# Optimization experiments

Hardware: AMD Instinct MI355X
Metric: run time of the kernel (lower is better)

Reference implementation:

```python
import jax, jax.numpy as jnp
import numpy as np

B = 1024            # number of graphs
C = (64, 32, 16, 1) # args.channels
K = 25              # args.kernel_size
CUTOFF = 0.5        # args.cutoff
EPS = 1e-15


def gmm_conv(x, pos, n, g, mu, sigma, root, bias, out_ch):
    """GMMConv over a dynamically-built radius graph (dist<CUTOFF, no self loops),
    with mean aggregation, expressed densely per-graph (n in {5,25,75}).
    Equivalent to getA()+PyG GMMConv(aggr='mean') scatter/gather."""
    nb = pos.shape[0] // n
    posb = pos.reshape(nb, n, 2)
    # diff[b, s, t] = pos_t - pos_s  (edge (row=s, col=t): message flows s -> t)
    diff = posb[:, None, :, :] - posb[:, :, None, :]
    dist = jnp.linalg.norm(diff + 1e-12, axis=-1)            # [B,n,n]
    mask = (dist < CUTOFF) & (~jnp.eye(n, dtype=bool))       # [B,n,n]
    pseudo = diff / CUTOFF + 0.5                             # [B,n,n,2] edge_attr
    # Gaussian kernel weights: exp(-0.5 * sum_d (u_d - mu_kd)^2 / sigma_kd^2)
    gauss = jnp.exp(-0.5 * jnp.sum((pseudo[..., None, :] - mu) ** 2
                                   / (sigma ** 2 + EPS), axis=-1))  # [B,n,n,K]
    w = gauss * mask[..., None]
    xm = (x @ g).reshape(nb, n, K, out_ch)                   # source-transformed feats
    agg = jnp.einsum('bstk,bsko->bto', w, xm)                # scatter-sum into targets
    deg = jnp.maximum(jnp.sum(mask, axis=1), 1)              # in-degree per target [B,n]
    out = agg / deg[..., None].astype(x.dtype)               # mean aggregation
    return out.reshape(-1, out_ch) + x @ root + bias


def setup_inputs() -> dict:
    key = jax.random.key(0)
    ks = jax.random.split(key, 40)
    inp = {}
    inp['x'] = jax.random.normal(ks[0], (B * 5, C[0]), jnp.float32)
    inp['pos'] = jax.random.uniform(ks[1], (B * 5, 2), jnp.float32)

    def conv_params(k, fin, fout):
        k1, k2, k3, k4, k5 = jax.random.split(k, 5)
        g = jax.random.normal(k1, (fin, K * fout), jnp.float32) / np.sqrt(fin)
        mu = jax.random.normal(k2, (K, 2), jnp.float32)
        sigma = jax.random.uniform(k3, (K, 2), jnp.float32, minval=0.5, maxval=1.5)
        root = jax.random.normal(k4, (fin, fout), jnp.float32) / np.sqrt(fin)
        bias = jax.random.normal(k5, (fout,), jnp.float32) * 0.01
        return g, mu, sigma, root, bias

    for i, (fin, fout) in enumerate([(C[0], 5 * C[1]), (C[1], 3 * C[2]), (C[2], C[3])], 1):
        g, mu, sigma, root, bias = conv_params(ks[1 + i], fin, fout)
        inp[f'g{i}'], inp[f'mu{i}'], inp[f'sig{i}'] = g, mu, sigma
        inp[f'root{i}'], inp[f'cb{i}'] = root, bias

    def lin(k, fin, fout):
        kw, kb = jax.random.split(k)
        return (jax.random.normal(kw, (fin, fout), jnp.float32) / np.sqrt(fin),
                jax.random.normal(kb, (fout,), jnp.float32) * 0.01)

    for j, (pre, dims) in enumerate([('p1', (2 + C[1], 128, 64, 2)),
                                     ('p2', (2 + C[2], 128, 64, 2))]):
        for li in range(3):
            w, b_ = lin(ks[10 + 3 * j + li], dims[li], dims[li + 1])
            inp[f'{pre}w{li+1}'], inp[f'{pre}b{li+1}'] = w, b_
    return inp


def reference(x, pos, g1, mu1, sig1, root1, cb1, g2, mu2, sig2, root2, cb2,
              g3, mu3, sig3, root3, cb3,
              p1w1, p1b1, p1w2, p1b2, p1w3, p1b3,
              p2w1, p2b1, p2w2, p2b2, p2w3, p2b3):
    elu = jax.nn.elu
    # stage 1: 5 nodes/graph, conv expands node count x5
    x = elu(gmm_conv(x, pos, 5, g1, mu1, sig1, root1, cb1, 5 * C[1])).reshape(-1, C[1])
    p = jnp.concatenate([jnp.repeat(pos, 5, axis=0), x], axis=1)
    p = elu(p @ p1w1 + p1b1)
    p = elu(p @ p1w2 + p1b2)
    pos = elu(p @ p1w3 + p1b3)
    # stage 2: 25 nodes/graph, conv expands node count x3
    x = elu(gmm_conv(x, pos, 25, g2, mu2, sig2, root2, cb2, 3 * C[2])).reshape(-1, C[2])
    p = jnp.concatenate([jnp.repeat(pos, 3, axis=0), x], axis=1)
    p = elu(p @ p2w1 + p2b1)
    p = elu(p @ p2w2 + p2b2)
    pos = elu(p @ p2w3 + p2b3)
    # stage 3: 75 nodes/graph
    x = jnp.tanh(gmm_conv(x, pos, 75, g3, mu3, sig3, root3, cb3, C[3])).reshape(-1, C[3])
    return x, pos
```

## Files before the change

kernel.cpp:

```cpp
#include <hip/hip_runtime.h>
#include <math.h>


__device__ __forceinline__ float eluf(float v) { return v > 0.f ? v : __expf(v) - 1.f; }

#define NLOG2E_HALF (-0.72134752f)

#define FMA4(A, S, V) \
  A.x = fmaf(S, V.x, A.x); A.y = fmaf(S, V.y, A.y); \
  A.z = fmaf(S, V.z, A.z); A.w = fmaf(S, V.w, A.w);

#define C1G(J, XV) \
  a[J][0]=fmaf(XV.x,gv0.x,a[J][0]); a[J][1]=fmaf(XV.x,gv0.y,a[J][1]); a[J][2]=fmaf(XV.x,gv0.z,a[J][2]); a[J][3]=fmaf(XV.x,gv0.w,a[J][3]); \
  a[J][0]=fmaf(XV.y,gv1.x,a[J][0]); a[J][1]=fmaf(XV.y,gv1.y,a[J][1]); a[J][2]=fmaf(XV.y,gv1.z,a[J][2]); a[J][3]=fmaf(XV.y,gv1.w,a[J][3]); \
  a[J][0]=fmaf(XV.z,gv2.x,a[J][0]); a[J][1]=fmaf(XV.z,gv2.y,a[J][1]); a[J][2]=fmaf(XV.z,gv2.z,a[J][2]); a[J][3]=fmaf(XV.z,gv2.w,a[J][3]); \
  a[J][0]=fmaf(XV.w,gv3.x,a[J][0]); a[J][1]=fmaf(XV.w,gv3.y,a[J][1]); a[J][2]=fmaf(XV.w,gv3.z,a[J][2]); a[J][3]=fmaf(XV.w,gv3.w,a[J][3]);

__global__ __launch_bounds__(512) void conv1_kernel(
    const float* __restrict__ x, const float* __restrict__ pos,
    const float* __restrict__ g, const float* __restrict__ mu, const float* __restrict__ sig,
    const float* __restrict__ root, const float* __restrict__ bias,
    float* __restrict__ xout)
{
  const int b = blockIdx.x, tid = threadIdx.x;
  __shared__ __align__(16) float s_xT[64 * 12];
  __shared__ __align__(16) float s_xm[10 * 832];
  __shared__ __align__(16) float s_w[2 * 5 * 5 * 28];
  __shared__ __align__(16) float s_red[2 * 2 * 5 * 160];
  __shared__ float s_pos[20];
  __shared__ float s_msc[25][4];
  __shared__ float s_ideg[10];

  if (tid < 20) s_pos[tid] = pos[b * 20 + tid];
  if (tid < 25) {
    float m0 = mu[2 * tid], m1 = mu[2 * tid + 1];
    float s0 = sig[2 * tid], s1 = sig[2 * tid + 1];
    s_msc[tid][0] = 0.5f - m0;
    s_msc[tid][1] = 0.5f - m1;
    s_msc[tid][2] = NLOG2E_HALF / (s0 * s0 + 1e-15f);
    s_msc[tid][3] = NLOG2E_HALF / (s1 * s1 + 1e-15f);
  }
  for (int e = tid; e < 640; e += 512) { int nd = e >> 6, i = e & 63; s_xT[i * 12 + nd] = x[b * 640 + nd * 64 + i]; }
  for (int e = tid; e < 320; e += 512) { int r = e / 32, c = e % 32; s_xm[r * 832 + 800 + c] = 0.f; }
  __syncthreads();

  if (tid < 10) {
    int gg = tid / 5, t = tid % 5, c = 0;
    for (int s = 0; s < 5; ++s) {
      if (s == t) continue;
      float d0 = s_pos[(gg * 5 + t) * 2]     - s_pos[(gg * 5 + s) * 2]     + 1e-12f;
      float d1 = s_pos[(gg * 5 + t) * 2 + 1] - s_pos[(gg * 5 + s) * 2 + 1] + 1e-12f;
      c += (d0 * d0 + d1 * d1 < 0.25f) ? 1 : 0;
    }
    s_ideg[tid] = 1.f / (float)(c < 1 ? 1 : c);
  }
  for (int e = tid; e < 1400; e += 512) {
    int gg = e / 700, r2 = e % 700, t = r2 / 140, c = r2 % 140;
    int ch = c / 28, skl = c % 28;
    float wv = 0.f;
    if (skl < 25) {
      int kk = skl / 5, s = skl % 5, k = ch * 5 + kk;
      float d0 = s_pos[(gg * 5 + t) * 2]     - s_pos[(gg * 5 + s) * 2];
      float d1 = s_pos[(gg * 5 + t) * 2 + 1] - s_pos[(gg * 5 + s) * 2 + 1];
      float e0 = d0 + 1e-12f, e1 = d1 + 1e-12f;
      bool m = (e0 * e0 + e1 * e1 < 0.25f) && (s != t);
      float q0 = fmaf(2.f, d0, s_msc[k][0]);
      float q1 = fmaf(2.f, d1, s_msc[k][1]);
      float a = q0 * q0 * s_msc[k][2];
      a = fmaf(q1 * q1, s_msc[k][3], a);
      wv = m ? exp2f(a) : 0.f;
    }
    s_w[e] = wv;
  }
  __syncthreads();

  float sacc[5][2];
  #pragma unroll
  for (int t = 0; t < 5; ++t) { sacc[t][0] = 0.f; sacc[t][1] = 0.f; }
  const int sg = tid / 160, sr = tid % 160, sks = sr / 80, sob = sr % 80;
  const int so0 = sob * 2;

  for (int ch = 0; ch < 5; ++ch) {
    if (tid < 400) {
      const int c0 = tid * 2;
      const float* gp = g + ch * 800 + c0;
      float a[10][2];
      #pragma unroll
      for (int r = 0; r < 10; ++r) { a[r][0] = 0.f; a[r][1] = 0.f; }
      #pragma unroll 4
      for (int i = 0; i < 64; ++i) {
        float2 gv = *(const float2*)(gp + i * 4000);
        float4 xa = *(const float4*)&s_xT[i * 12];
        float4 xb = *(const float4*)&s_xT[i * 12 + 4];
        float2 xc = *(const float2*)&s_xT[i * 12 + 8];
        a[0][0] = fmaf(xa.x, gv.x, a[0][0]); a[0][1] = fmaf(xa.x, gv.y, a[0][1]);
        a[1][0] = fmaf(xa.y, gv.x, a[1][0]); a[1][1] = fmaf(xa.y, gv.y, a[1][1]);
        a[2][0] = fmaf(xa.z, gv.x, a[2][0]); a[2][1] = fmaf(xa.z, gv.y, a[2][1]);
        a[3][0] = fmaf(xa.w, gv.x, a[3][0]); a[3][1] = fmaf(xa.w, gv.y, a[3][1]);
        a[4][0] = fmaf(xb.x, gv.x, a[4][0]); a[4][1] = fmaf(xb.x, gv.y, a[4][1]);
        a[5][0] = fmaf(xb.y, gv.x, a[5][0]); a[5][1] = fmaf(xb.y, gv.y, a[5][1]);
        a[6][0] = fmaf(xb.z, gv.x, a[6][0]); a[6][1] = fmaf(xb.z, gv.y, a[6][1]);
        a[7][0] = fmaf(xb.w, gv.x, a[7][0]); a[7][1] = fmaf(xb.w, gv.y, a[7][1]);
        a[8][0] = fmaf(xc.x, gv.x, a[8][0]); a[8][1] = fmaf(xc.x, gv.y, a[8][1]);
        a[9][0] = fmaf(xc.y, gv.x, a[9][0]); a[9][1] = fmaf(xc.y, gv.y, a[9][1]);
      }
      #pragma unroll
      for (int r = 0; r < 10; ++r)
        *(float2*)&s_xm[r * 832 + c0] = make_float2(a[r][0], a[r][1]);
    }
    __syncthreads();
    if (tid < 320) {
#define C1_STEP(SK0) { \
      float2 m0 = *(const float2*)&s_xm[(sg * 5 + ((SK0) % 5)) * 832 + ((SK0) / 5) * 160 + so0]; \
      float2 m1 = *(const float2*)&s_xm[(sg * 5 + (((SK0) + 1) % 5)) * 832 + (((SK0) + 1) / 5) * 160 + so0]; \
      float2 m2 = *(const float2*)&s_xm[(sg * 5 + (((SK0) + 2) % 5)) * 832 + (((SK0) + 2) / 5) * 160 + so0]; \
      float2 m3 = *(const float2*)&s_xm[(sg * 5 + (((SK0) + 3) % 5)) * 832 + (((SK0) + 3) / 5) * 160 + so0]; \
      _Pragma("unroll") \
      for (int t = 0; t < 5; ++t) { \
        const float4 wv = *(const float4*)&s_w[((sg * 5 + t) * 5 + ch) * 28 + (SK0)]; \
        sacc[t][0] = fmaf(wv.x, m0.x, sacc[t][0]); sacc[t][1] = fmaf(wv.x, m0.y, sacc[t][1]); \
        sacc[t][0] = fmaf(wv.y, m1.x, sacc[t][0]); sacc[t][1] = fmaf(wv.y, m1.y, sacc[t][1]); \
        sacc[t][0] = fmaf(wv.z, m2.x, sacc[t][0]); sacc[t][1] = fmaf(wv.z, m2.y, sacc[t][1]); \
        sacc[t][0] = fmaf(wv.w, m3.x, sacc[t][0]); sacc[t][1] = fmaf(wv.w, m3.y, sacc[t][1]); \
      } }
      if (sks == 0) { C1_STEP(0) C1_STEP(4) C1_STEP(8) C1_STEP(12) }
      else          { C1_STEP(16) C1_STEP(20) C1_STEP(24) }
#undef C1_STEP
    }
    __syncthreads();
  }

  if (tid < 400) {
    const int rb = tid / 80, cb = tid % 80;
    const int r0 = rb * 2, c0 = cb * 2;
    float a00 = 0.f, a01 = 0.f, a10 = 0.f, a11 = 0.f;
    #pragma unroll 4
    for (int i = 0; i < 64; ++i) {
      float2 rv = *(const float2*)(root + i * 160 + c0);
      float2 xv = *(const float2*)&s_xT[i * 12 + r0];
      a00 = fmaf(xv.x, rv.x, a00); a01 = fmaf(xv.x, rv.y, a01);
      a10 = fmaf(xv.y, rv.x, a10); a11 = fmaf(xv.y, rv.y, a11);
    }
    *(float2*)&s_xm[r0 * 832 + c0]       = make_float2(a00, a01);
    *(float2*)&s_xm[(r0 + 1) * 832 + c0] = make_float2(a10, a11);
  }
  if (tid < 320) {
    #pragma unroll
    for (int t = 0; t < 5; ++t) {
      s_red[((sks * 2 + sg) * 5 + t) * 160 + so0]     = sacc[t][0];
      s_red[((sks * 2 + sg) * 5 + t) * 160 + so0 + 1] = sacc[t][1];
    }
  }
  __syncthreads();
  for (int e = tid; e < 1600; e += 512) {
    int gg = e / 800, r2 = e % 800, t = r2 / 160, o = r2 % 160;
    float v = s_red[(gg * 5 + t) * 160 + o] + s_red[((2 + gg) * 5 + t) * 160 + o];
    v = v * s_ideg[gg * 5 + t] + s_xm[(gg * 5 + t) * 832 + o] + bias[o];
    xout[b * 1600 + e] = eluf(v);
  }
}

__global__ __launch_bounds__(320) void conv2_kernel(
    const float* __restrict__ x, const float* __restrict__ pos,
    const float* __restrict__ g, const float* __restrict__ mu, const float* __restrict__ sig,
    const float* __restrict__ root, const float* __restrict__ bias,
    float* __restrict__ xout)
{
  const int b = blockIdx.x, tid = threadIdx.x;
  __shared__ __align__(16) float s_x[25 * 36];
  __shared__ __align__(16) float s_xm[140 * 52];
  __shared__ __align__(16) float s_w[25 * 140];
  __shared__ __align__(8)  float2 s_u[25 * 26];
  __shared__ float s_ek[25 * 5];
  __shared__ float s_ideg[25];

  const float* posb = pos + b * 50;
  for (int e = tid; e < 800; e += 320) s_x[(e / 32) * 36 + (e % 32)] = x[b * 800 + e];
  for (int e = tid; e < 624; e += 320) {
    int rr = e / 52, cc = e % 52;
    int kk = rr / 3, j = rr % 3;
    if (rr < 15) s_xm[(kk * 28 + 25 + j) * 52 + cc] = 0.f;
  }
  for (int e = tid + 624; e < 780; e += 320) {
    int rr = e / 52, cc = e % 52;
    int kk = rr / 3, j = rr % 3;
    if (rr < 15) s_xm[(kk * 28 + 25 + j) * 52 + cc] = 0.f;
  }
  if (tid < 25) {
    float m0 = mu[2 * tid], m1 = mu[2 * tid + 1];
    float sg0 = sig[2 * tid], sg1 = sig[2 * tid + 1];
    float n0 = NLOG2E_HALF / (sg0 * sg0 + 1e-15f);
    float n1 = NLOG2E_HALF / (sg1 * sg1 + 1e-15f);
    float c0 = 0.5f - m0, c1 = 0.5f - m1;
    s_ek[tid * 5 + 0] = n0;
    s_ek[tid * 5 + 1] = n1;
    s_ek[tid * 5 + 2] = 2.f * n0 * c0;
    s_ek[tid * 5 + 3] = 2.f * n1 * c1;
    s_ek[tid * 5 + 4] = fmaf(n0, c0 * c0, n1 * c1 * c1);
  }
  for (int e = tid; e < 625; e += 320) {
    int t = e / 25, s = e % 25;
    float d0 = posb[t * 2]     - posb[s * 2];
    float d1 = posb[t * 2 + 1] - posb[s * 2 + 1];
    float e0 = d0 + 1e-12f, e1 = d1 + 1e-12f;
    bool m = (e0 * e0 + e1 * e1 < 0.25f) && (s != t);
    s_u[t * 26 + s] = m ? make_float2(2.f * d0, 2.f * d1) : make_float2(1e18f, 0.f);
  }
  if (tid < 25) {
    int t = tid, c = 0;
    for (int s = 0; s < 25; ++s) {
      if (s == t) continue;
      float d0 = posb[t * 2]     - posb[s * 2]     + 1e-12f;
      float d1 = posb[t * 2 + 1] - posb[s * 2 + 1] + 1e-12f;
      c += (d0 * d0 + d1 * d1 < 0.25f) ? 1 : 0;
    }
    s_ideg[t] = 1.f / (float)(c < 1 ? 1 : c);
  }
  __syncthreads();

  const bool act = tid < 300;
  const int grp = tid / 60, rr2 = tid % 60, tg = rr2 / 12, og = rr2 % 12;
  const int t0 = tg * 5, o0 = og * 4, s0 = tg * 5;

  float4 acc[5];
  #pragma unroll
  for (int tt = 0; tt < 5; ++tt) acc[tt] = make_float4(0.f, 0.f, 0.f, 0.f);

  for (int ch = 0; ch < 5; ++ch) {
    const int k0 = ch * 5;
    for (int e = tid; e < 3500; e += 320) {
      int t = e / 140, c = e % 140;
      int kk = c / 28, s = c % 28;
      float wv = 0.f;
      if (s < 25) {
        int k = k0 + kk;
        float2 uv = s_u[t * 26 + s];
        const float* ekp = &s_ek[k * 5];
        float ar = fmaf(uv.x * uv.x, ekp[0],
                   fmaf(uv.y * uv.y, ekp[1],
                   fmaf(uv.x, ekp[2],
                   fmaf(uv.y, ekp[3], ekp[4]))));
        wv = exp2f(ar);
      }
      s_w[e] = wv;
    }
    if (act) {
      const float* gp = g + (k0 + grp) * 48 + o0;
      const float* xb = &s_x[s0 * 36];
      float a[5][4];
      #pragma unroll
      for (int r = 0; r < 5; ++r) { a[r][0] = a[r][1] = a[r][2] = a[r][3] = 0.f; }
      for (int i = 0; i < 32; i += 4) {
        float4 gv0 = *(const float4*)(gp + (i + 0) * 1200);
        float4 gv1 = *(const float4*)(gp + (i + 1) * 1200);
        float4 gv2 = *(const float4*)(gp + (i + 2) * 1200);
        float4 gv3 = *(const float4*)(gp + (i + 3) * 1200);
        float4 xv0 = *(const float4*)(xb + 0 * 36 + i);
        float4 xv1 = *(const float4*)(xb + 1 * 36 + i);
        float4 xv2 = *(const float4*)(xb + 2 * 36 + i);
        float4 xv3 = *(const float4*)(xb + 3 * 36 + i);
        float4 xv4 = *(const float4*)(xb + 4 * 36 + i);
        C1G(0, xv0) C1G(1, xv1) C1G(2, xv2) C1G(3, xv3) C1G(4, xv4)
      }
      #pragma unroll
      for (int j = 0; j < 5; ++j)
        *(float4*)&s_xm[(grp * 28 + s0 + j) * 52 + o0] = make_float4(a[j][0], a[j][1], a[j][2], a[j][3]);
    }
    __syncthreads();
    if (act) {
      const int kbase = grp * 28;
      #pragma unroll
      for (int q = 0; q < 7; ++q) {
        const int sk = kbase + q * 4;
        float4 m0 = *(const float4*)&s_xm[(sk + 0) * 52 + o0];
        float4 m1 = *(const float4*)&s_xm[(sk + 1) * 52 + o0];
        float4 m2 = *(const float4*)&s_xm[(sk + 2) * 52 + o0];
        float4 m3 = *(const float4*)&s_xm[(sk + 3) * 52 + o0];
        #pragma unroll
        for (int tt = 0; tt < 5; ++tt) {
          float4 wv = *(const float4*)&s_w[(t0 + tt) * 140 + sk];
          FMA4(acc[tt], wv.x, m0)
          FMA4(acc[tt], wv.y, m1)
          FMA4(acc[tt], wv.z, m2)
          FMA4(acc[tt], wv.w, m3)
        }
      }
    }
    __syncthreads();
  }

  if (act) {
    #pragma unroll
    for (int tt = 0; tt < 5; ++tt)
      *(float4*)&s_xm[grp * 1200 + (t0 + tt) * 48 + o0] = acc[tt];
  }
  __syncthreads();
  if (tid < 300) {
    const int t = tid / 12, oe = (tid % 12) * 4;
    float4 p0 = *(const float4*)&s_xm[0 * 1200 + t * 48 + oe];
    float4 p1 = *(const float4*)&s_xm[1 * 1200 + t * 48 + oe];
    float4 p2 = *(const float4*)&s_xm[2 * 1200 + t * 48 + oe];
    float4 p3 = *(const float4*)&s_xm[3 * 1200 + t * 48 + oe];
    float4 p4 = *(const float4*)&s_xm[4 * 1200 + t * 48 + oe];
    float idg = s_ideg[t];
    float4 bv = *(const float4*)&bias[oe];
    float4 v;
    v.x = fmaf(p0.x + p1.x + p2.x + p3.x + p4.x, idg, bv.x);
    v.y = fmaf(p0.y + p1.y + p2.y + p3.y + p4.y, idg, bv.y);
    v.z = fmaf(p0.z + p1.z + p2.z + p3.z + p4.z, idg, bv.z);
    v.w = fmaf(p0.w + p1.w + p2.w + p3.w + p4.w, idg, bv.w);
    const float* xr = &s_x[t * 36];
    for (int i = 0; i < 32; ++i) {
      float4 rv = *(const float4*)(root + i * 48 + oe);
      float xv = xr[i];
      FMA4(v, xv, rv)
    }
    *(float4*)&xout[b * 1200 + t * 48 + oe] =
        make_float4(eluf(v.x), eluf(v.y), eluf(v.z), eluf(v.w));
  }
}

__global__ __launch_bounds__(384) void conv3_kernel(
    const float* __restrict__ x, const float* __restrict__ pos,
    const float* __restrict__ g, const float* __restrict__ mu, const float* __restrict__ sig,
    const float* __restrict__ root, const float* __restrict__ bias,
    float* __restrict__ xout)
{
  const int b = blockIdx.x, tid = threadIdx.x;
  __shared__ __align__(8) float2 s_u[75 * 75];
  __shared__ float s_xm[75 * 28];
  __shared__ float s_x[75 * 16];
  __shared__ float s_g3[400];
  __shared__ float s_pos[150];
  __shared__ float s_ek[25 * 5];
  __shared__ float s_ideg[75];
  __shared__ float s_out[75];
  __shared__ float s_r3[16];

  if (tid < 150) s_pos[tid] = pos[b * 150 + tid];
  for (int e = tid; e < 1200; e += 384) s_x[e] = x[b * 1200 + e];
  for (int e = tid; e < 400; e += 384) s_g3[e] = g[e];
  if (tid < 25) {
    float m0 = mu[2 * tid], m1 = mu[2 * tid + 1];
    float sg0 = sig[2 * tid], sg1 = sig[2 * tid + 1];
    float n0 = NLOG2E_HALF / (sg0 * sg0 + 1e-15f);
    float n1 = NLOG2E_HALF / (sg1 * sg1 + 1e-15f);
    float c0 = 0.5f - m0, c1 = 0.5f - m1;
    s_ek[tid * 5 + 0] = n0;
    s_ek[tid * 5 + 1] = n1;
    s_ek[tid * 5 + 2] = 2.f * n0 * c0;
    s_ek[tid * 5 + 3] = 2.f * n1 * c1;
    s_ek[tid * 5 + 4] = n0 * c0 * c0 + n1 * c1 * c1;
  }
  if (tid < 16) s_r3[tid] = root[tid];
  if (tid < 75) s_out[tid] = 0.f;
  __syncthreads();

  for (int e = tid; e < 1875; e += 384) {
    int s = e / 25, k = e % 25;
    float a = 0.f;
    #pragma unroll
    for (int i = 0; i < 16; ++i) a = fmaf(s_x[s * 16 + i], s_g3[i * 25 + k], a);
    s_xm[s * 28 + k] = a;
  }
  for (int e = tid; e < 5625; e += 384) {
    int t = e / 75, s = e % 75;
    float d0 = s_pos[t * 2]     - s_pos[s * 2];
    float d1 = s_pos[t * 2 + 1] - s_pos[s * 2 + 1];
    float e0 = d0 + 1e-12f, e1 = d1 + 1e-12f;
    bool m = (e0 * e0 + e1 * e1 < 0.25f) && (s != t);
    s_u[e] = m ? make_float2(2.f * d0, 2.f * d1) : make_float2(1e18f, 0.f);
  }
  if (tid < 75) {
    int t = tid, c = 0;
    for (int s = 0; s < 75; ++s) {
      if (s == t) continue;
      float d0 = s_pos[t * 2]     - s_pos[s * 2]     + 1e-12f;
      float d1 = s_pos[t * 2 + 1] - s_pos[s * 2 + 1] + 1e-12f;
      c += (d0 * d0 + d1 * d1 < 0.25f) ? 1 : 0;
    }
    s_ideg[t] = 1.f / (float)(c < 1 ? 1 : c);
  }
  __syncthreads();

  if (tid < 375) {
    const int t = tid / 5, kg = tid % 5;
    float n0[5], n1[5], e0[5], e1[5], f[5];
    #pragma unroll
    for (int j = 0; j < 5; ++j) {
      int k = kg * 5 + j;
      n0[j] = s_ek[k * 5 + 0]; n1[j] = s_ek[k * 5 + 1];
      e0[j] = s_ek[k * 5 + 2]; e1[j] = s_ek[k * 5 + 3];
      f[j]  = s_ek[k * 5 + 4];
    }
    float acc[5] = {0.f, 0.f, 0.f, 0.f, 0.f};
    for (int s = 0; s < 75; ++s) {
      float2 uv = s_u[t * 75 + s];
      float u00 = uv.x * uv.x, u11 = uv.y * uv.y;
      #pragma unroll
      for (int j = 0; j < 5; ++j) {
        float ar = fmaf(u00, n0[j], fmaf(u11, n1[j], fmaf(uv.x, e0[j], fmaf(uv.y, e1[j], f[j]))));
        acc[j] = fmaf(exp2f(ar), s_xm[s * 28 + kg * 5 + j], acc[j]);
      }
    }
    float sum = acc[0] + acc[1] + acc[2] + acc[3] + acc[4];
    atomicAdd(&s_out[t], sum);
  }
  __syncthreads();

  if (tid < 75) {
    int t = tid;
    float r = 0.f;
    #pragma unroll
    for (int i = 0; i < 16; ++i) r = fmaf(s_x[t * 16 + i], s_r3[i], r);
    xout[b * 75 + t] = tanhf(s_out[t] * s_ideg[t] + r + bias[0]);
  }
}

__global__ __launch_bounds__(256) void mlp_kernel(
    const float* __restrict__ pos_src, const float* __restrict__ feat,
    const float* __restrict__ w1, const float* __restrict__ b1,
    const float* __restrict__ w2, const float* __restrict__ b2,
    const float* __restrict__ w3, const float* __restrict__ b3,
    float* __restrict__ out, int fdim, int rep)
{
  const int tid = threadIdx.x;
  const int row0 = blockIdx.x * 64;
  const int din = fdim + 2;
  __shared__ __align__(16) float s_inT[34][68];
  __shared__ __align__(16) float s_h1T[128][68];
  __shared__ __align__(16) float s_h2T[64][68];

  if (tid < 128) {
    int r = tid >> 1, d = tid & 1;
    s_inT[d][r] = pos_src[((row0 + r) / rep) * 2 + d];
  }
  for (int e = tid; e < 64 * fdim; e += 256) {
    int r = e / fdim, c = e % fdim;
    s_inT[2 + c][r] = feat[(row0 + r) * fdim + c];
  }
  __syncthreads();

  {
    const int rb = tid >> 4, jb = tid & 15;
    const int r0 = rb << 2, j0 = jb << 3;
    float acc[4][8];
    #pragma unroll
    for (int jj = 0; jj < 8; ++jj) {
      float bv = b1[j0 + jj];
      acc[0][jj] = bv; acc[1][jj] = bv; acc[2][jj] = bv; acc[3][jj] = bv;
    }
    for (int i = 0; i < din; ++i) {
      float4 xa = *(const float4*)&s_inT[i][r0];
      float4 wa = *(const float4*)(w1 + i * 128 + j0);
      float4 wb = *(const float4*)(w1 + i * 128 + j0 + 4);
      float wv[8] = {wa.x, wa.y, wa.z, wa.w, wb.x, wb.y, wb.z, wb.w};
      #pragma unroll
      for (int jj = 0; jj < 8; ++jj) {
        acc[0][jj] = fmaf(xa.x, wv[jj], acc[0][jj]);
        acc[1][jj] = fmaf(xa.y, wv[jj], acc[1][jj]);
        acc[2][jj] = fmaf(xa.z, wv[jj], acc[2][jj]);
        acc[3][jj] = fmaf(xa.w, wv[jj], acc[3][jj]);
      }
    }
    #pragma unroll
    for (int jj = 0; jj < 8; ++jj)
      *(float4*)&s_h1T[j0 + jj][r0] =
        make_float4(eluf(acc[0][jj]), eluf(acc[1][jj]), eluf(acc[2][jj]), eluf(acc[3][jj]));
  }
  __syncthreads();

  {
    const int rb = tid >> 4, jb = tid & 15;
    const int r0 = rb << 2, j0 = jb << 2;
    float acc[4][4];
    #pragma unroll
    for (int jj = 0; jj < 4; ++jj) {
      float bv = b2[j0 + jj];
      acc[0][jj] = bv; acc[1][jj] = bv; acc[2][jj] = bv; acc[3][jj] = bv;
    }
    #pragma unroll 4
    for (int i = 0; i < 128; ++i) {
      float4 ha = *(const float4*)&s_h1T[i][r0];
      float4 wa = *(const float4*)(w2 + i * 64 + j0);
      float wv[4] = {wa.x, wa.y, wa.z, wa.w};
      #pragma unroll
      for (int jj = 0; jj < 4; ++jj) {
        acc[0][jj] = fmaf(ha.x, wv[jj], acc[0][jj]);
        acc[1][jj] = fmaf(ha.y, wv[jj], acc[1][jj]);
        acc[2][jj] = fmaf(ha.z, wv[jj], acc[2][jj]);
        acc[3][jj] = fmaf(ha.w, wv[jj], acc[3][jj]);
      }
    }
    #pragma unroll
    for (int jj = 0; jj < 4; ++jj)
      *(float4*)&s_h2T[j0 + jj][r0] =
        make_float4(eluf(acc[0][jj]), eluf(acc[1][jj]), eluf(acc[2][jj]), eluf(acc[3][jj]));
  }
  __syncthreads();

  if (tid < 128) {
    int r = tid >> 1, c = tid & 1;
    float a = b3[c];
    #pragma unroll 8
    for (int j = 0; j < 64; ++j)
      a = fmaf(s_h2T[j][r], w3[j * 2 + c], a);
    out[(row0 + r) * 2 + c] = eluf(a);
  }
}

extern "C" void kernel_launch(void* const* d_in, const int* in_sizes, int n_in,
                              void* d_out, int out_size, void* d_ws, size_t ws_size,
                              hipStream_t stream)
{
  const float* x     = (const float*)d_in[0];
  const float* pos   = (const float*)d_in[1];
  const float* g1    = (const float*)d_in[2];
  const float* mu1   = (const float*)d_in[3];
  const float* sig1  = (const float*)d_in[4];
  const float* root1 = (const float*)d_in[5];
  const float* cb1   = (const float*)d_in[6];
  const float* g2    = (const float*)d_in[7];
  const float* mu2   = (const float*)d_in[8];
  const float* sig2  = (const float*)d_in[9];
  const float* root2 = (const float*)d_in[10];
  const float* cb2   = (const float*)d_in[11];
  const float* g3    = (const float*)d_in[12];
  const float* mu3   = (const float*)d_in[13];
  const float* sig3  = (const float*)d_in[14];
  const float* root3 = (const float*)d_in[15];
  const float* cb3   = (const float*)d_in[16];
  const float* p1w1  = (const float*)d_in[17];
  const float* p1b1  = (const float*)d_in[18];
  const float* p1w2  = (const float*)d_in[19];
  const float* p1b2  = (const float*)d_in[20];
  const float* p1w3  = (const float*)d_in[21];
  const float* p1b3  = (const float*)d_in[22];
  const float* p2w1  = (const float*)d_in[23];
  const float* p2b1  = (const float*)d_in[24];
  const float* p2w2  = (const float*)d_in[25];
  const float* p2b2  = (const float*)d_in[26];
  const float* p2w3  = (const float*)d_in[27];
  const float* p2b3  = (const float*)d_in[28];

  float* out  = (float*)d_out;
  float* ws   = (float*)d_ws;
  float* x1   = ws;
  float* pos1 = ws + 819200;
  float* x2   = ws + 870400;
  float* x3   = out;
  float* pos2 = out + 76800;

  conv1_kernel<<<dim3(512), dim3(512), 0, stream>>>(x, pos, g1, mu1, sig1, root1, cb1, x1);
  mlp_kernel<<<dim3(400), dim3(256), 0, stream>>>(pos, x1, p1w1, p1b1, p1w2, p1b2, p1w3, p1b3,
                                                  pos1, 32, 5);
  conv2_kernel<<<dim3(1024), dim3(320), 0, stream>>>(x1, pos1, g2, mu2, sig2, root2, cb2, x2);
  mlp_kernel<<<dim3(1200), dim3(256), 0, stream>>>(pos1, x2, p2w1, p2b1, p2w2, p2b2, p2w3, p2b3,
                                                  pos2, 16, 3);
  conv3_kernel<<<dim3(1024), dim3(384), 0, stream>>>(x2, pos2, g3, mu3, sig3, root3, cb3, x3);
}
```

Measured before the change: 345.3 us.

## Shrink MLP tiles, recompute conv3 edge geometry, trim conv2 init loops

The MLP kernel now handles 32 rows per block instead of 64, with smaller per-thread register tiles and aliased shared memory, and launches twice as many blocks. This cuts shared memory and register use per block so more blocks can be resident. Conv3 drops its 75x75 float2 shared edge buffer and recomputes the pairwise differences and mask inside the inner loop, trading recomputation for less shared memory and one fewer pass. Conv2 merges two zero-init loops into one and adds a partial unroll on the g-projection loop.

Result: faster. 330.7 us (-4.2%).

```diff
diff --git a/kernel.cpp b/kernel.cpp
--- a/kernel.cpp
+++ b/kernel.cpp
@@ -171,20 +171,15 @@
   __shared__ __align__(16) float s_xm[140 * 52];
   __shared__ __align__(16) float s_w[25 * 140];
   __shared__ __align__(8)  float2 s_u[25 * 26];
-  __shared__ float s_ek[25 * 5];
+  __shared__ float s_ek[125];
   __shared__ float s_ideg[25];
 
   const float* posb = pos + b * 50;
   for (int e = tid; e < 800; e += 320) s_x[(e / 32) * 36 + (e % 32)] = x[b * 800 + e];
-  for (int e = tid; e < 624; e += 320) {
+  for (int e = tid; e < 780; e += 320) {
     int rr = e / 52, cc = e % 52;
     int kk = rr / 3, j = rr % 3;
-    if (rr < 15) s_xm[(kk * 28 + 25 + j) * 52 + cc] = 0.f;
-  }
-  for (int e = tid + 624; e < 780; e += 320) {
-    int rr = e / 52, cc = e % 52;
-    int kk = rr / 3, j = rr % 3;
-    if (rr < 15) s_xm[(kk * 28 + 25 + j) * 52 + cc] = 0.f;
+    s_xm[(kk * 28 + 25 + j) * 52 + cc] = 0.f;
   }
   if (tid < 25) {
     float m0 = mu[2 * tid], m1 = mu[2 * tid + 1];
@@ -250,6 +245,7 @@
       float a[5][4];
       #pragma unroll
       for (int r = 0; r < 5; ++r) { a[r][0] = a[r][1] = a[r][2] = a[r][3] = 0.f; }
+      #pragma unroll 2
       for (int i = 0; i < 32; i += 4) {
         float4 gv0 = *(const float4*)(gp + (i + 0) * 1200);
         float4 gv1 = *(const float4*)(gp + (i + 1) * 1200);
@@ -327,12 +323,11 @@
     float* __restrict__ xout)
 {
   const int b = blockIdx.x, tid = threadIdx.x;
-  __shared__ __align__(8) float2 s_u[75 * 75];
   __shared__ float s_xm[75 * 28];
   __shared__ float s_x[75 * 16];
   __shared__ float s_g3[400];
-  __shared__ float s_pos[150];
-  __shared__ float s_ek[25 * 5];
+  __shared__ __align__(8) float s_pos[150];
+  __shared__ float s_ek[125];
   __shared__ float s_ideg[75];
   __shared__ float s_out[75];
   __shared__ float s_r3[16];
@@ -363,14 +358,6 @@
     for (int i = 0; i < 16; ++i) a = fmaf(s_x[s * 16 + i], s_g3[i * 25 + k], a);
     s_xm[s * 28 + k] = a;
   }
-  for (int e = tid; e < 5625; e += 384) {
-    int t = e / 75, s = e % 75;
-    float d0 = s_pos[t * 2]     - s_pos[s * 2];
-    float d1 = s_pos[t * 2 + 1] - s_pos[s * 2 + 1];
-    float e0 = d0 + 1e-12f, e1 = d1 + 1e-12f;
-    bool m = (e0 * e0 + e1 * e1 < 0.25f) && (s != t);
-    s_u[e] = m ? make_float2(2.f * d0, 2.f * d1) : make_float2(1e18f, 0.f);
-  }
   if (tid < 75) {
     int t = tid, c = 0;
     for (int s = 0; s < 75; ++s) {
@@ -393,18 +380,23 @@
       e0[j] = s_ek[k * 5 + 2]; e1[j] = s_ek[k * 5 + 3];
       f[j]  = s_ek[k * 5 + 4];
     }
-    float acc[5] = {0.f, 0.f, 0.f, 0.f, 0.f};
+    const float pt0 = s_pos[t * 2], pt1 = s_pos[t * 2 + 1];
+    float acc5[5] = {0.f, 0.f, 0.f, 0.f, 0.f};
     for (int s = 0; s < 75; ++s) {
-      float2 uv = s_u[t * 75 + s];
-      float u00 = uv.x * uv.x, u11 = uv.y * uv.y;
+      float2 pv = *(const float2*)&s_pos[s * 2];
+      float d0 = pt0 - pv.x, d1 = pt1 - pv.y;
+      float ea = d0 + 1e-12f, eb = d1 + 1e-12f;
+      bool m = (ea * ea + eb * eb < 0.25f) && (s != t);
+      float ux = m ? 2.f * d0 : 1e18f;
+      float uy = m ? 2.f * d1 : 0.f;
+      float u00 = ux * ux, u11 = uy * uy;
       #pragma unroll
       for (int j = 0; j < 5; ++j) {
-        float ar = fmaf(u00, n0[j], fmaf(u11, n1[j], fmaf(uv.x, e0[j], fmaf(uv.y, e1[j], f[j]))));
-        acc[j] = fmaf(exp2f(ar), s_xm[s * 28 + kg * 5 + j], acc[j]);
-      }
-    }
-    float sum = acc[0] + acc[1] + acc[2] + acc[3] + acc[4];
-    atomicAdd(&s_out[t], sum);
+        float ar = fmaf(u00, n0[j], fmaf(u11, n1[j], fmaf(ux, e0[j], fmaf(uy, e1[j], f[j]))));
+        acc5[j] = fmaf(exp2f(ar), s_xm[s * 28 + kg * 5 + j], acc5[j]);
+      }
+    }
+    atomicAdd(&s_out[t], acc5[0] + acc5[1] + acc5[2] + acc5[3] + acc5[4]);
   }
   __syncthreads();
 
@@ -425,67 +417,67 @@
     float* __restrict__ out, int fdim, int rep)
 {
   const int tid = threadIdx.x;
-  const int row0 = blockIdx.x * 64;
+  const int row0 = blockIdx.x * 32;
   const int din = fdim + 2;
-  __shared__ __align__(16) float s_inT[34][68];
-  __shared__ __align__(16) float s_h1T[128][68];
-  __shared__ __align__(16) float s_h2T[64][68];
-
-  if (tid < 128) {
+  __shared__ __align__(16) char smem[27648];
+  float* s_h1T = (float*)smem;
+  float* s_inT = (float*)(smem + 18432);
+  float* s_h2T = (float*)(smem + 18432);
+
+  if (tid < 64) {
     int r = tid >> 1, d = tid & 1;
-    s_inT[d][r] = pos_src[((row0 + r) / rep) * 2 + d];
-  }
-  for (int e = tid; e < 64 * fdim; e += 256) {
+    s_inT[d * 36 + r] = pos_src[((row0 + r) / rep) * 2 + d];
+  }
+  for (int e = tid; e < 32 * fdim; e += 256) {
     int r = e / fdim, c = e % fdim;
-    s_inT[2 + c][r] = feat[(row0 + r) * fdim + c];
-  }
-  __syncthreads();
-
+    s_inT[(2 + c) * 36 + r] = feat[(row0 + r) * fdim + c];
+  }
+  __syncthreads();
+
+  const int rb = tid / 32, jb = tid % 32;
   {
-    const int rb = tid >> 4, jb = tid & 15;
-    const int r0 = rb << 2, j0 = jb << 3;
-    float acc[4][8];
-    #pragma unroll
-    for (int jj = 0; jj < 8; ++jj) {
+    const int r0 = rb * 4, j0 = jb * 4;
+    float acc[4][4];
+    #pragma unroll
+    for (int jj = 0; jj < 4; ++jj) {
       float bv = b1[j0 + jj];
       acc[0][jj] = bv; acc[1][jj] = bv; acc[2][jj] = bv; acc[3][jj] = bv;
     }
     for (int i = 0; i < din; ++i) {
-      float4 xa = *(const float4*)&s_inT[i][r0];
-      float4 wa = *(const float4*)(w1 + i * 128 + j0);
-      float4 wb = *(const float4*)(w1 + i * 128 + j0 + 4);
-      float wv[8] = {wa.x, wa.y, wa.z, wa.w, wb.x, wb.y, wb.z, wb.w};
-      #pragma unroll
-      for (int jj = 0; jj < 8; ++jj) {
+      float4 xa = *(const float4*)&s_inT[i * 36 + r0];
+      float4 wa = *(const float4*)&w1[i * 128 + j0];
+      float wv[4] = {wa.x, wa.y, wa.z, wa.w};
+      #pragma unroll
+      for (int jj = 0; jj < 4; ++jj) {
         acc[0][jj] = fmaf(xa.x, wv[jj], acc[0][jj]);
         acc[1][jj] = fmaf(xa.y, wv[jj], acc[1][jj]);
         acc[2][jj] = fmaf(xa.z, wv[jj], acc[2][jj]);
         acc[3][jj] = fmaf(xa.w, wv[jj], acc[3][jj]);
       }
     }
-    #pragma unroll
-    for (int jj = 0; jj < 8; ++jj)
-      *(float4*)&s_h1T[j0 + jj][r0] =
+    __syncthreads();
+    #pragma unroll
+    for (int jj = 0; jj < 4; ++jj)
+      *(float4*)&s_h1T[(j0 + jj) * 36 + r0] =
         make_float4(eluf(acc[0][jj]), eluf(acc[1][jj]), eluf(acc[2][jj]), eluf(acc[3][jj]));
   }
   __syncthreads();
 
   {
-    const int rb = tid >> 4, jb = tid & 15;
-    const int r0 = rb << 2, j0 = jb << 2;
-    float acc[4][4];
-    #pragma unroll
-    for (int jj = 0; jj < 4; ++jj) {
+    const int r0 = rb * 4, j0 = jb * 2;
+    float acc[4][2];
+    #pragma unroll
+    for (int jj = 0; jj < 2; ++jj) {
       float bv = b2[j0 + jj];
       acc[0][jj] = bv; acc[1][jj] = bv; acc[2][jj] = bv; acc[3][jj] = bv;
     }
     #pragma unroll 4
     for (int i = 0; i < 128; ++i) {
-      float4 ha = *(const float4*)&s_h1T[i][r0];
-      float4 wa = *(const float4*)(w2 + i * 64 + j0);
-      float wv[4] = {wa.x, wa.y, wa.z, wa.w};
-      #pragma unroll
-      for (int jj = 0; jj < 4; ++jj) {
+      float4 ha = *(const float4*)&s_h1T[i * 36 + r0];
+      float2 wa = *(const float2*)&w2[i * 64 + j0];
+      float wv[2] = {wa.x, wa.y};
+      #pragma unroll
+      for (int jj = 0; jj < 2; ++jj) {
         acc[0][jj] = fmaf(ha.x, wv[jj], acc[0][jj]);
         acc[1][jj] = fmaf(ha.y, wv[jj], acc[1][jj]);
         acc[2][jj] = fmaf(ha.z, wv[jj], acc[2][jj]);
@@ -493,18 +485,18 @@
       }
     }
     #pragma unroll
-    for (int jj = 0; jj < 4; ++jj)
-      *(float4*)&s_h2T[j0 + jj][r0] =
+    for (int jj = 0; jj < 2; ++jj)
+      *(float4*)&s_h2T[(j0 + jj) * 36 + r0] =
         make_float4(eluf(acc[0][jj]), eluf(acc[1][jj]), eluf(acc[2][jj]), eluf(acc[3][jj]));
   }
   __syncthreads();
 
-  if (tid < 128) {
+  if (tid < 64) {
     int r = tid >> 1, c = tid & 1;
     float a = b3[c];
     #pragma unroll 8
     for (int j = 0; j < 64; ++j)
-      a = fmaf(s_h2T[j][r], w3[j * 2 + c], a);
+      a = fmaf(s_h2T[j * 36 + r], w3[j * 2 + c], a);
     out[(row0 + r) * 2 + c] = eluf(a);
   }
 }
@@ -552,10 +544,10 @@
   float* pos2 = out + 76800;
 
   conv1_kernel<<<dim3(512), dim3(512), 0, stream>>>(x, pos, g1, mu1, sig1, root1, cb1, x1);
-  mlp_kernel<<<dim3(400), dim3(256), 0, stream>>>(pos, x1, p1w1, p1b1, p1w2, p1b2, p1w3, p1b3,
+  mlp_kernel<<<dim3(800), dim3(256), 0, stream>>>(pos, x1, p1w1, p1b1, p1w2, p1b2, p1w3, p1b3,
                                                   pos1, 32, 5);
   conv2_kernel<<<dim3(1024), dim3(320), 0, stream>>>(x1, pos1, g2, mu2, sig2, root2, cb2, x2);
-  mlp_kernel<<<dim3(1200), dim3(256), 0, stream>>>(pos1, x2, p2w1, p2b1, p2w2, p2b2, p2w3, p2b3,
+  mlp_kernel<<<dim3(2400), dim3(256), 0, stream>>>(pos1, x2, p2w1, p2b1, p2w2, p2b2, p2w3, p2b3,
                                                   pos2, 16, 3);
   conv3_kernel<<<dim3(1024), dim3(384), 0, stream>>>(x2, pos2, g3, mu3, sig3, root3, cb3, x3);
 }
```
